# Kernel optimization log

Hardware: AMD Instinct MI355X
Metric: run time of the kernel (lower is better)

## Reference

```python
import jax, jax.numpy as jnp
import numpy as np

NUM_HEADS = 12

def setup_inputs() -> dict:
    key = jax.random.key(0)
    k1, k2, k3 = jax.random.split(key, 3)
    B, T, H = 2, 2048, 768
    x = jax.random.normal(k1, (B, T, H), dtype=jnp.float32)
    attn_mask = jnp.ones((B, T), dtype=jnp.int32)
    Wqkv = jax.random.normal(k2, (H, 3 * H), dtype=jnp.float32) * 0.02
    bqkv = jnp.zeros((3 * H,), dtype=jnp.float32)
    Wproj = jax.random.normal(k3, (H, H), dtype=jnp.float32) * 0.02
    bproj = jnp.zeros((H,), dtype=jnp.float32)
    return {"x": x, "attn_mask": attn_mask, "Wqkv": Wqkv, "bqkv": bqkv,
            "Wproj": Wproj, "bproj": bproj}

def reference(x, attn_mask, Wqkv, bqkv, Wproj, bproj):
    B, T, H = x.shape
    nh = NUM_HEADS
    hd = H // nh
    qkv = x @ Wqkv + bqkv                      # [B,T,3H]
    q, k, v = jnp.split(qkv, 3, axis=-1)
    # [B,T,H] -> [B,nh,T,hd]
    def heads(t):
        return t.reshape(B, T, nh, hd).transpose(0, 2, 1, 3)
    q, k, v = heads(q), heads(k), heads(v)
    scores = jnp.einsum('bhqd,bhkd->bhqk', q, k) / jnp.sqrt(jnp.float32(hd))
    causal = jnp.tril(jnp.ones((T, T), dtype=bool))          # allowed positions
    key_ok = attn_mask.astype(bool)[:, None, None, :]        # [B,1,1,T]
    allowed = causal[None, None] & key_ok
    scores = jnp.where(allowed, scores, -jnp.inf)
    weights = jax.nn.softmax(scores, axis=-1)                # dropout=0 (eval)
    out = jnp.einsum('bhqk,bhkd->bhqd', weights, v)
    out = out.transpose(0, 2, 1, 3).reshape(B, T, H)
    return out @ Wproj + bproj
```

## Files before the change

### kernel.cpp

```cpp
#include <hip/hip_runtime.h>
#include <stdint.h>

typedef unsigned short u16;
typedef unsigned int   u32;
typedef unsigned char  u8;
typedef __attribute__((ext_vector_type(8))) short short8;
typedef __attribute__((ext_vector_type(4))) float f32x4;
typedef __attribute__((ext_vector_type(4))) unsigned short u16x4;

#define DEV static __device__ __forceinline__

static constexpr int Bc = 2, Tc = 2048, Hc = 768, NH = 12, HD = 64;
static constexpr int BTc = Bc * Tc;
static constexpr int N3 = 3 * Hc;
static constexpr int NBH = Bc * NH;
static constexpr int NITEMS = 32 * NBH;
static constexpr float QSCALE = 0.125f * 1.44269504088896f;

DEV u16 f2bf(float f) {
  u32 u = __float_as_uint(f);
  u32 r = (u + 0x7fffu + ((u >> 16) & 1u)) >> 16;
  return (u16)r;
}

DEV float fexp2(float x) {
#if __has_builtin(__builtin_amdgcn_exp2f)
  return __builtin_amdgcn_exp2f(x);
#else
  return exp2f(x);
#endif
}

DEV u32 cvtpk_bf16(float lo, float hi) {
  u32 r;
  asm("v_cvt_pk_bf16_f32 %0, %1, %2" : "=v"(r) : "v"(lo), "v"(hi));
  return r;
}

DEV void gl_lds16(const u16* g, u16* l) {
  __builtin_amdgcn_global_load_lds(
      (const __attribute__((address_space(1))) u32*)g,
      (__attribute__((address_space(3))) u32*)l, 16, 0, 0);
}

#define MFMA(a, b, c) __builtin_amdgcn_mfma_f32_16x16x32_bf16((a), (b), (c), 0, 0, 0)

__global__ void k_cvt(const float4* __restrict__ in, uint4* __restrict__ out, int n8,
                      const int* __restrict__ mask, u8* __restrict__ flags,
                      u32* __restrict__ ctr) {
  if (blockIdx.x == 0 && threadIdx.x < 64) {
    int t = threadIdx.x;
    if (t == 0) *ctr = 0;
    int b = t >> 5, kb = t & 31;
    const int* m = mask + b * Tc + kb * 64;
    int all = 1;
    for (int i = 0; i < 64; ++i) all &= (m[i] != 0);
    flags[b * 32 + kb] = (u8)all;
  }
  int i = blockIdx.x * 256 + threadIdx.x;
  if (i >= n8) return;
  float4 a = in[2 * i], b = in[2 * i + 1];
  uint4 o;
  o.x = f2bf(a.x) | ((u32)f2bf(a.y) << 16);
  o.y = f2bf(a.z) | ((u32)f2bf(a.w) << 16);
  o.z = f2bf(b.x) | ((u32)f2bf(b.y) << 16);
  o.w = f2bf(b.z) | ((u32)f2bf(b.w) << 16);
  out[i] = o;
}

__global__ __launch_bounds__(256) void k_transpose_w(const float* __restrict__ in,
                                                     u16* __restrict__ out, int R, int C) {
  __shared__ u16 tile[64][65];
  int c0 = blockIdx.x * 64, r0 = blockIdx.y * 64;
  int tx = threadIdx.x, ty = threadIdx.y;
  for (int i = ty; i < 64; i += 4)
    tile[i][tx] = f2bf(in[(size_t)(r0 + i) * C + c0 + tx]);
  __syncthreads();
  for (int i = ty; i < 64; i += 4)
    out[(size_t)(c0 + i) * R + r0 + tx] = tile[tx][i];
}

template <int EPI>
__global__ __launch_bounds__(256) void k_gemm(const u16* __restrict__ A,
                                              const u16* __restrict__ BTm,
                                              const float* __restrict__ bias,
                                              u16* __restrict__ oQ, u16* __restrict__ oK,
                                              u16* __restrict__ oV, float* __restrict__ oF,
                                              int M, int N, int K) {
  __shared__ u16 As[128 * 32];
  __shared__ u16 Bs[128 * 32];
  const int tid = threadIdx.x;
  const int lane = tid & 63, wave = tid >> 6;
  const int wr = wave >> 1, wc = wave & 1;
  const int row0 = blockIdx.y * 128, col0 = blockIdx.x * 128;

  f32x4 acc[4][4];
#pragma unroll
  for (int m = 0; m < 4; ++m)
#pragma unroll
    for (int n = 0; n < 4; ++n) acc[m][n] = (f32x4)(0.f);

  const int srow = lane >> 2;
  const int sg = lane & 3;
  const int sf = (lane >> 3) & 3;
  const int kfetch = ((sg ^ sf) * 8);

  const int r16 = lane & 15;
  const int g = lane >> 4;
  const int fr = (r16 >> 1) & 3;
  const int koff = ((g ^ fr) * 8);

  for (int k0 = 0; k0 < K; k0 += 32) {
    if (k0) __syncthreads();
#pragma unroll
    for (int p = 0; p < 2; ++p) {
      int seg = wave * 2 + p;
      int row = seg * 16 + srow;
      gl_lds16(A + (size_t)(row0 + row) * K + k0 + kfetch, &As[seg * 512 + lane * 8]);
      gl_lds16(BTm + (size_t)(col0 + row) * K + k0 + kfetch, &Bs[seg * 512 + lane * 8]);
    }
    __syncthreads();
    short8 af[4], bf[4];
#pragma unroll
    for (int m = 0; m < 4; ++m)
      af[m] = *(const short8*)&As[(wr * 64 + m * 16 + r16) * 32 + koff];
#pragma unroll
    for (int n = 0; n < 4; ++n)
      bf[n] = *(const short8*)&Bs[(wc * 64 + n * 16 + r16) * 32 + koff];
#pragma unroll
    for (int m = 0; m < 4; ++m)
#pragma unroll
      for (int n = 0; n < 4; ++n)
        acc[m][n] = MFMA(af[m], bf[n], acc[m][n]);
  }

#pragma unroll
  for (int m = 0; m < 4; ++m) {
    int rowg = row0 + wr * 64 + m * 16 + g * 4;
#pragma unroll
    for (int n = 0; n < 4; ++n) {
      int colg = col0 + wc * 64 + n * 16 + r16;
      float bv = bias[colg];
      if constexpr (EPI == 0) {
        int which = colg / Hc;
        int hc = colg - which * Hc;
        int h = hc >> 6, d = hc & 63;
        int b = rowg >> 11, t0 = rowg & 2047;
        if (which == 2) {
          u16x4 pk;
#pragma unroll
          for (int r = 0; r < 4; ++r) pk[r] = f2bf(acc[m][n][r] + bv);
          *(u16x4*)&oV[((size_t)(b * NH + h) * HD + d) * Tc + t0] = pk;
        } else {
#pragma unroll
          for (int r = 0; r < 4; ++r) {
            float v = acc[m][n][r] + bv;
            size_t dst = ((size_t)(b * NH + h) * Tc + t0 + r) * HD + d;
            if (which == 0) oQ[dst] = f2bf(v * QSCALE);
            else            oK[dst] = f2bf(v);
          }
        }
      } else {
#pragma unroll
        for (int r = 0; r < 4; ++r)
          oF[(size_t)(rowg + r) * Hc + colg] = acc[m][n][r] + bv;
      }
    }
  }
}

__global__ __launch_bounds__(256) void k_attn(const u16* __restrict__ Qh,
                                              const u16* __restrict__ Kh,
                                              const u16* __restrict__ VT,
                                              const int* __restrict__ mask,
                                              const u8* __restrict__ flags,
                                              u16* __restrict__ O,
                                              u32* __restrict__ ctr) {
  __shared__ u16 Ks[4][4096];
  __shared__ u16 Vs[4][4096];
  __shared__ u16 Ps[4][1024];
  __shared__ int s_item;
  const int tid = threadIdx.x, lane = tid & 63, wave = tid >> 6;
  const int r16 = lane & 15, g = lane >> 4;
  const int r7 = r16 & 7;
  const int skey = lane >> 3;
  const int sgr = lane & 7;
  const int sgd = ((sgr ^ skey) * 8);

  const int off0 = r16 * 64 + ((g ^ r7) * 8);
  const int off1 = r16 * 64 + (((4 + g) ^ r7) * 8);
  const int pwb = r16 * 32 + 2 * (g & 1);
  const int pgs = g >> 1;

  for (;;) {
    if (tid == 0) s_item = (int)atomicAdd(ctr, 1u);
    __syncthreads();
    const int item = s_item;
    if (item >= NITEMS) break;
    const int qt = 31 - item / NBH;
    const int bh = item % NBH;
    const int b = bh / NH, h = bh - b * NH;
    const int q0 = qt * 64;
    const int nt = qt + 1;
    const int qg = q0 + wave * 16 + r16;
    const int* mrow = mask + b * Tc;
    const u8* frow = flags + b * 32;

    const u16* qbase = Qh + ((size_t)bh * Tc + qg) * HD;
    const short8 qf0 = *(const short8*)(qbase + g * 8);
    const short8 qf1 = *(const short8*)(qbase + 32 + g * 8);

    f32x4 acc[4];
#pragma unroll
    for (int n = 0; n < 4; ++n) acc[n] = (f32x4)(0.f);
    float mrun = -3.0e38f, lrun = 0.f;

#pragma unroll
    for (int p = 0; p < 2; ++p) {
      int seg = wave * 2 + p;
      int rloc = seg * 8 + skey;
      gl_lds16(Kh + ((size_t)bh * Tc + rloc) * HD + sgd, &Ks[0][seg * 512 + lane * 8]);
      gl_lds16(VT + ((size_t)bh * HD + rloc) * Tc + sgd, &Vs[0][seg * 512 + lane * 8]);
    }
    if (nt > 1) {
#pragma unroll
      for (int p = 0; p < 2; ++p) {
        int seg = wave * 2 + p;
        int rloc = seg * 8 + skey;
        gl_lds16(Kh + ((size_t)bh * Tc + 64 + rloc) * HD + sgd, &Ks[1][seg * 512 + lane * 8]);
        gl_lds16(VT + ((size_t)bh * HD + rloc) * Tc + 64 + sgd, &Vs[1][seg * 512 + lane * 8]);
      }
    }

    for (int t = 0; t < nt; ++t) {
      const int kb = t * 64;
      const int rem = nt - 1 - t;

      if (rem >= 2) {
        const int kb2 = kb + 128;
        const int sp = (t + 2) & 3;
#pragma unroll
        for (int p = 0; p < 2; ++p) {
          int seg = wave * 2 + p;
          int rloc = seg * 8 + skey;
          gl_lds16(Kh + ((size_t)bh * Tc + kb2 + rloc) * HD + sgd,
                   &Ks[sp][seg * 512 + lane * 8]);
          gl_lds16(VT + ((size_t)bh * HD + rloc) * Tc + kb2 + sgd,
                   &Vs[sp][seg * 512 + lane * 8]);
        }
      }

      if (rem >= 2)      asm volatile("s_waitcnt vmcnt(8)" ::: "memory");
      else if (rem == 1) asm volatile("s_waitcnt vmcnt(4)" ::: "memory");
      else               asm volatile("s_waitcnt vmcnt(0)" ::: "memory");
      __builtin_amdgcn_sched_barrier(0);
      __builtin_amdgcn_s_barrier();
      __builtin_amdgcn_sched_barrier(0);

      const u16* Kc = &Ks[t & 3][0];
      const u16* Vc = &Vs[t & 3][0];

      f32x4 s[4];
#pragma unroll
      for (int n = 0; n < 4; ++n) {
        short8 kf0 = *(const short8*)&Kc[n * 1024 + off0];
        short8 kf1 = *(const short8*)&Kc[n * 1024 + off1];
        f32x4 z = (f32x4)(0.f);
        z = MFMA(kf0, qf0, z);
        z = MFMA(kf1, qf1, z);
        s[n] = z;
      }

      const bool diag = (t == nt - 1);
      if (diag || !frow[t]) {
        const int fl = frow[t];
#pragma unroll
        for (int n = 0; n < 4; ++n)
#pragma unroll
          for (int r = 0; r < 4; ++r) {
            int keyg = kb + n * 16 + g * 4 + r;
            bool ok = fl ? true : (mrow[keyg] != 0);
            if (diag) ok = ok && (keyg <= qg);
            if (!ok) s[n][r] = -3.0e38f;
          }
      }

      float lm;
      {
        float m0 = fmaxf(fmaxf(s[0][0], s[0][1]), fmaxf(s[0][2], s[0][3]));
        float m1 = fmaxf(fmaxf(s[1][0], s[1][1]), fmaxf(s[1][2], s[1][3]));
        float m2 = fmaxf(fmaxf(s[2][0], s[2][1]), fmaxf(s[2][2], s[2][3]));
        float m3 = fmaxf(fmaxf(s[3][0], s[3][1]), fmaxf(s[3][2], s[3][3]));
        lm = fmaxf(fmaxf(m0, m1), fmaxf(m2, m3));
      }
      if (!__all(lm <= mrun + 8.0f)) {
        float rm = fmaxf(lm, __shfl_xor(lm, 16));
        rm = fmaxf(rm, __shfl_xor(rm, 32));
        float nm = fmaxf(mrun, rm);
        float alpha = fexp2(mrun - nm);
        mrun = nm;
        lrun *= alpha;
#pragma unroll
        for (int r = 0; r < 4; ++r) {
          float ar = __shfl(alpha, g * 4 + r);
          acc[0][r] *= ar;
          acc[1][r] *= ar;
          acc[2][r] *= ar;
          acc[3][r] *= ar;
        }
      }
      float rs = 0.f;
#pragma unroll
      for (int n = 0; n < 4; ++n)
#pragma unroll
        for (int r = 0; r < 4; ++r) {
          float p = fexp2(s[n][r] - mrun);
          s[n][r] = p;
          rs += p;
        }
      lrun += rs;

      u32* pw = (u32*)&Ps[wave][0];
#pragma unroll
      for (int n = 0; n < 4; ++n) {
        u32 lo = cvtpk_bf16(s[n][0], s[n][1]);
        u32 hi = cvtpk_bf16(s[n][2], s[n][3]);
        int idx = pwb + (((2 * n + pgs) ^ r7) * 4);
        *(uint2*)&pw[idx] = make_uint2(lo, hi);
      }
      asm volatile("s_waitcnt lgkmcnt(0)" ::: "memory");
      const u16* pwr = &Ps[wave][0];
      short8 pa0 = *(const short8*)&pwr[off0];
      short8 pa1 = *(const short8*)&pwr[off1];

#pragma unroll
      for (int n = 0; n < 4; ++n) {
        short8 vf0 = *(const short8*)&Vc[n * 1024 + off0];
        short8 vf1 = *(const short8*)&Vc[n * 1024 + off1];
        acc[n] = MFMA(pa0, vf0, acc[n]);
        acc[n] = MFMA(pa1, vf1, acc[n]);
      }
      __builtin_amdgcn_sched_barrier(0);
    }

    float lt = lrun + __shfl_xor(lrun, 16);
    lt += __shfl_xor(lt, 32);
#pragma unroll
    for (int r = 0; r < 4; ++r) {
      int qr = q0 + wave * 16 + g * 4 + r;
      float inv = 1.0f / __shfl(lt, g * 4 + r);
      u16* orow = O + ((size_t)(b * Tc + qr)) * Hc + h * 64;
#pragma unroll
      for (int n = 0; n < 4; ++n) orow[n * 16 + r16] = f2bf(acc[n][r] * inv);
    }
  }
}

extern "C" void kernel_launch(void* const* d_in, const int* in_sizes, int n_in,
                              void* d_out, int out_size, void* d_ws, size_t ws_size,
                              hipStream_t stream) {
  const float* x = (const float*)d_in[0];
  const int* mask = (const int*)d_in[1];
  const float* Wqkv = (const float*)d_in[2];
  const float* bqkv = (const float*)d_in[3];
  const float* Wproj = (const float*)d_in[4];
  const float* bproj = (const float*)d_in[5];
  float* out = (float*)d_out;

  char* ws = (char*)d_ws;
  size_t off = 0;
  auto alloc = [&](size_t bytes) {
    char* p = ws + off;
    off += (bytes + 255) & ~(size_t)255;
    return p;
  };
  u16* xb     = (u16*)alloc((size_t)BTc * Hc * 2);
  u16* WqkvT  = (u16*)alloc((size_t)N3 * Hc * 2);
  u16* WprojT = (u16*)alloc((size_t)Hc * Hc * 2);
  u16* Qh     = (u16*)alloc((size_t)BTc * Hc * 2);
  u16* Kh     = (u16*)alloc((size_t)BTc * Hc * 2);
  u16* VT     = (u16*)alloc((size_t)BTc * Hc * 2);
  u32* ctr    = (u32*)alloc(256);
  u8*  flags  = (u8*)alloc(256);
  u16* Ob     = xb;

  int n8 = BTc * Hc / 8;
  k_cvt<<<(n8 + 255) / 256, 256, 0, stream>>>((const float4*)x, (uint4*)xb, n8,
                                              mask, flags, ctr);
  k_transpose_w<<<dim3(N3 / 64, Hc / 64), dim3(64, 4), 0, stream>>>(Wqkv, WqkvT, Hc, N3);
  k_transpose_w<<<dim3(Hc / 64, Hc / 64), dim3(64, 4), 0, stream>>>(Wproj, WprojT, Hc, Hc);
  k_gemm<0><<<dim3(N3 / 128, BTc / 128), 256, 0, stream>>>(xb, WqkvT, bqkv, Qh, Kh, VT,
                                                           nullptr, BTc, N3, Hc);
  k_attn<<<dim3(512), 256, 0, stream>>>(Qh, Kh, VT, mask, flags, Ob, ctr);
  k_gemm<1><<<dim3(Hc / 128, BTc / 128), 256, 0, stream>>>(Ob, WprojT, bproj, nullptr,
                                                           nullptr, nullptr, out, BTc, Hc, Hc);
}
```

Before: 112.9 us.

## Split attention key tiles across wave pairs and merge partial softmax states

The attention kernel moves from 256 to 512 threads per block. Each pair of waves now shares a 16-row query group and splits every 64-key tile into two 32-key halves, each wave computing its half of the scores and PV product. At the end the two partial results (running max, sum, accumulator) are combined through shared memory. The aim is more waves in flight per block and a shorter dependent chain per wave, at the cost of an extra merge step with two barriers and more register and LDS pressure. It also adds s_setprio around the MFMA sections.

Result: faster. 107.1 us (-5.1%).

```diff
diff --git a/kernel.cpp b/kernel.cpp
--- a/kernel.cpp
+++ b/kernel.cpp
@@ -16,6 +16,8 @@
 static constexpr int NBH = Bc * NH;
 static constexpr int NITEMS = 32 * NBH;
 static constexpr float QSCALE = 0.125f * 1.44269504088896f;
+static constexpr float MRINIT = -1.0e38f;
+static constexpr float SMASK  = -3.0e38f;
 
 DEV u16 f2bf(float f) {
   u32 u = __float_as_uint(f);
@@ -169,18 +171,20 @@
   }
 }
 
-__global__ __launch_bounds__(256) void k_attn(const u16* __restrict__ Qh,
-                                              const u16* __restrict__ Kh,
-                                              const u16* __restrict__ VT,
-                                              const int* __restrict__ mask,
-                                              const u8* __restrict__ flags,
-                                              u16* __restrict__ O,
-                                              u32* __restrict__ ctr) {
+__global__ __launch_bounds__(512, 4) void k_attn(const u16* __restrict__ Qh,
+                                                 const u16* __restrict__ Kh,
+                                                 const u16* __restrict__ VT,
+                                                 const int* __restrict__ mask,
+                                                 const u8* __restrict__ flags,
+                                                 u16* __restrict__ O,
+                                                 u32* __restrict__ ctr) {
   __shared__ u16 Ks[4][4096];
   __shared__ u16 Vs[4][4096];
-  __shared__ u16 Ps[4][1024];
+  __shared__ u16 Ps[8][512];
   __shared__ int s_item;
   const int tid = threadIdx.x, lane = tid & 63, wave = tid >> 6;
+  const int qgrp = wave >> 1;
+  const int kh = wave & 1;
   const int r16 = lane & 15, g = lane >> 4;
   const int r7 = r16 & 7;
   const int skey = lane >> 3;
@@ -189,8 +193,8 @@
 
   const int off0 = r16 * 64 + ((g ^ r7) * 8);
   const int off1 = r16 * 64 + (((4 + g) ^ r7) * 8);
-  const int pwb = r16 * 32 + 2 * (g & 1);
-  const int pgs = g >> 1;
+  const int offv = kh ? off1 : off0;
+  const int prd = r16 * 16 + ((g ^ (r16 & 3)) << 2);
 
   for (;;) {
     if (tid == 0) s_item = (int)atomicAdd(ctr, 1u);
@@ -202,7 +206,7 @@
     const int b = bh / NH, h = bh - b * NH;
     const int q0 = qt * 64;
     const int nt = qt + 1;
-    const int qg = q0 + wave * 16 + r16;
+    const int qg = q0 + qgrp * 16 + r16;
     const int* mrow = mask + b * Tc;
     const u8* frow = flags + b * 32;
 
@@ -213,22 +217,15 @@
     f32x4 acc[4];
 #pragma unroll
     for (int n = 0; n < 4; ++n) acc[n] = (f32x4)(0.f);
-    float mrun = -3.0e38f, lrun = 0.f;
-
-#pragma unroll
-    for (int p = 0; p < 2; ++p) {
-      int seg = wave * 2 + p;
-      int rloc = seg * 8 + skey;
-      gl_lds16(Kh + ((size_t)bh * Tc + rloc) * HD + sgd, &Ks[0][seg * 512 + lane * 8]);
-      gl_lds16(VT + ((size_t)bh * HD + rloc) * Tc + sgd, &Vs[0][seg * 512 + lane * 8]);
-    }
-    if (nt > 1) {
-#pragma unroll
-      for (int p = 0; p < 2; ++p) {
-        int seg = wave * 2 + p;
-        int rloc = seg * 8 + skey;
-        gl_lds16(Kh + ((size_t)bh * Tc + 64 + rloc) * HD + sgd, &Ks[1][seg * 512 + lane * 8]);
-        gl_lds16(VT + ((size_t)bh * HD + rloc) * Tc + 64 + sgd, &Vs[1][seg * 512 + lane * 8]);
+    float mrun = MRINIT, lrun = 0.f;
+
+    {
+      int rloc = wave * 8 + skey;
+      gl_lds16(Kh + ((size_t)bh * Tc + rloc) * HD + sgd, &Ks[0][wave * 512 + lane * 8]);
+      gl_lds16(VT + ((size_t)bh * HD + rloc) * Tc + sgd, &Vs[0][wave * 512 + lane * 8]);
+      if (nt > 1) {
+        gl_lds16(Kh + ((size_t)bh * Tc + 64 + rloc) * HD + sgd, &Ks[1][wave * 512 + lane * 8]);
+        gl_lds16(VT + ((size_t)bh * HD + rloc) * Tc + 64 + sgd, &Vs[1][wave * 512 + lane * 8]);
       }
     }
 
@@ -239,19 +236,15 @@
       if (rem >= 2) {
         const int kb2 = kb + 128;
         const int sp = (t + 2) & 3;
-#pragma unroll
-        for (int p = 0; p < 2; ++p) {
-          int seg = wave * 2 + p;
-          int rloc = seg * 8 + skey;
-          gl_lds16(Kh + ((size_t)bh * Tc + kb2 + rloc) * HD + sgd,
-                   &Ks[sp][seg * 512 + lane * 8]);
-          gl_lds16(VT + ((size_t)bh * HD + rloc) * Tc + kb2 + sgd,
-                   &Vs[sp][seg * 512 + lane * 8]);
-        }
-      }
-
-      if (rem >= 2)      asm volatile("s_waitcnt vmcnt(8)" ::: "memory");
-      else if (rem == 1) asm volatile("s_waitcnt vmcnt(4)" ::: "memory");
+        int rloc = wave * 8 + skey;
+        gl_lds16(Kh + ((size_t)bh * Tc + kb2 + rloc) * HD + sgd,
+                 &Ks[sp][wave * 512 + lane * 8]);
+        gl_lds16(VT + ((size_t)bh * HD + rloc) * Tc + kb2 + sgd,
+                 &Vs[sp][wave * 512 + lane * 8]);
+      }
+
+      if (rem >= 2)      asm volatile("s_waitcnt vmcnt(4)" ::: "memory");
+      else if (rem == 1) asm volatile("s_waitcnt vmcnt(2)" ::: "memory");
       else               asm volatile("s_waitcnt vmcnt(0)" ::: "memory");
       __builtin_amdgcn_sched_barrier(0);
       __builtin_amdgcn_s_barrier();
@@ -260,28 +253,31 @@
       const u16* Kc = &Ks[t & 3][0];
       const u16* Vc = &Vs[t & 3][0];
 
-      f32x4 s[4];
-#pragma unroll
-      for (int n = 0; n < 4; ++n) {
-        short8 kf0 = *(const short8*)&Kc[n * 1024 + off0];
-        short8 kf1 = *(const short8*)&Kc[n * 1024 + off1];
+      f32x4 s[2];
+      __builtin_amdgcn_s_setprio(1);
+#pragma unroll
+      for (int np = 0; np < 2; ++np) {
+        const int ng = 2 * kh + np;
+        short8 kf0 = *(const short8*)&Kc[ng * 1024 + off0];
+        short8 kf1 = *(const short8*)&Kc[ng * 1024 + off1];
         f32x4 z = (f32x4)(0.f);
         z = MFMA(kf0, qf0, z);
         z = MFMA(kf1, qf1, z);
-        s[n] = z;
-      }
+        s[np] = z;
+      }
+      __builtin_amdgcn_s_setprio(0);
 
       const bool diag = (t == nt - 1);
       if (diag || !frow[t]) {
         const int fl = frow[t];
 #pragma unroll
-        for (int n = 0; n < 4; ++n)
+        for (int np = 0; np < 2; ++np)
 #pragma unroll
           for (int r = 0; r < 4; ++r) {
-            int keyg = kb + n * 16 + g * 4 + r;
+            int keyg = kb + 16 * (2 * kh + np) + 4 * g + r;
             bool ok = fl ? true : (mrow[keyg] != 0);
             if (diag) ok = ok && (keyg <= qg);
-            if (!ok) s[n][r] = -3.0e38f;
+            if (!ok) s[np][r] = SMASK;
           }
       }
 
@@ -289,9 +285,7 @@
       {
         float m0 = fmaxf(fmaxf(s[0][0], s[0][1]), fmaxf(s[0][2], s[0][3]));
         float m1 = fmaxf(fmaxf(s[1][0], s[1][1]), fmaxf(s[1][2], s[1][3]));
-        float m2 = fmaxf(fmaxf(s[2][0], s[2][1]), fmaxf(s[2][2], s[2][3]));
-        float m3 = fmaxf(fmaxf(s[3][0], s[3][1]), fmaxf(s[3][2], s[3][3]));
-        lm = fmaxf(fmaxf(m0, m1), fmaxf(m2, m3));
+        lm = fmaxf(m0, m1);
       }
       if (!__all(lm <= mrun + 8.0f)) {
         float rm = fmaxf(lm, __shfl_xor(lm, 16));
@@ -311,47 +305,74 @@
       }
       float rs = 0.f;
 #pragma unroll
-      for (int n = 0; n < 4; ++n)
+      for (int np = 0; np < 2; ++np)
 #pragma unroll
         for (int r = 0; r < 4; ++r) {
-          float p = fexp2(s[n][r] - mrun);
-          s[n][r] = p;
+          float p = fexp2(s[np][r] - mrun);
+          s[np][r] = p;
           rs += p;
         }
       lrun += rs;
 
       u32* pw = (u32*)&Ps[wave][0];
 #pragma unroll
+      for (int np = 0; np < 2; ++np) {
+        u32 lo = cvtpk_bf16(s[np][0], s[np][1]);
+        u32 hi = cvtpk_bf16(s[np][2], s[np][3]);
+        int kg = 2 * np + (g >> 1);
+        int idx = r16 * 16 + ((kg ^ (r16 & 3)) << 2) + 2 * (g & 1);
+        *(uint2*)&pw[idx] = make_uint2(lo, hi);
+      }
+      short8 pa = *(const short8*)&pw[prd];
+
+      __builtin_amdgcn_s_setprio(1);
+#pragma unroll
       for (int n = 0; n < 4; ++n) {
-        u32 lo = cvtpk_bf16(s[n][0], s[n][1]);
-        u32 hi = cvtpk_bf16(s[n][2], s[n][3]);
-        int idx = pwb + (((2 * n + pgs) ^ r7) * 4);
-        *(uint2*)&pw[idx] = make_uint2(lo, hi);
-      }
-      asm volatile("s_waitcnt lgkmcnt(0)" ::: "memory");
-      const u16* pwr = &Ps[wave][0];
-      short8 pa0 = *(const short8*)&pwr[off0];
-      short8 pa1 = *(const short8*)&pwr[off1];
-
-#pragma unroll
-      for (int n = 0; n < 4; ++n) {
-        short8 vf0 = *(const short8*)&Vc[n * 1024 + off0];
-        short8 vf1 = *(const short8*)&Vc[n * 1024 + off1];
-        acc[n] = MFMA(pa0, vf0, acc[n]);
-        acc[n] = MFMA(pa1, vf1, acc[n]);
-      }
+        short8 vf = *(const short8*)&Vc[n * 1024 + offv];
+        acc[n] = MFMA(pa, vf, acc[n]);
+      }
+      __builtin_amdgcn_s_setprio(0);
       __builtin_amdgcn_sched_barrier(0);
     }
 
     float lt = lrun + __shfl_xor(lrun, 16);
     lt += __shfl_xor(lt, 32);
-#pragma unroll
-    for (int r = 0; r < 4; ++r) {
-      int qr = q0 + wave * 16 + g * 4 + r;
-      float inv = 1.0f / __shfl(lt, g * 4 + r);
-      u16* orow = O + ((size_t)(b * Tc + qr)) * Hc + h * 64;
-#pragma unroll
-      for (int n = 0; n < 4; ++n) orow[n * 16 + r16] = f2bf(acc[n][r] * inv);
+
+    __syncthreads();
+    float* ab = (float*)&Ks[0][0] + qgrp * 1024;
+    float* ml = (float*)&Ps[0][0];
+    if (kh == 1) {
+#pragma unroll
+      for (int n = 0; n < 4; ++n)
+#pragma unroll
+        for (int r = 0; r < 4; ++r)
+          ab[(4 * g + r) * 64 + 16 * n + r16] = acc[n][r];
+      if (g == 0) {
+        ml[qgrp * 32 + r16 * 2]     = mrun;
+        ml[qgrp * 32 + r16 * 2 + 1] = lt;
+      }
+    }
+    __syncthreads();
+    if (kh == 0) {
+#pragma unroll
+      for (int r = 0; r < 4; ++r) {
+        int q = 4 * g + r;
+        float mA = __shfl(mrun, q);
+        float lA = __shfl(lt, q);
+        float mB = ml[qgrp * 32 + q * 2];
+        float lB = ml[qgrp * 32 + q * 2 + 1];
+        float ms = fmaxf(mA, mB);
+        float cA = fexp2(mA - ms);
+        float cB = fexp2(mB - ms);
+        float linv = 1.0f / (lA * cA + lB * cB);
+        int qr = q0 + qgrp * 16 + q;
+        u16* orow = O + ((size_t)(b * Tc + qr)) * Hc + h * 64;
+#pragma unroll
+        for (int n = 0; n < 4; ++n) {
+          float v = (acc[n][r] * cA + ab[q * 64 + 16 * n + r16] * cB) * linv;
+          orow[n * 16 + r16] = f2bf(v);
+        }
+      }
     }
   }
 }
@@ -391,7 +412,7 @@
   k_transpose_w<<<dim3(Hc / 64, Hc / 64), dim3(64, 4), 0, stream>>>(Wproj, WprojT, Hc, Hc);
   k_gemm<0><<<dim3(N3 / 128, BTc / 128), 256, 0, stream>>>(xb, WqkvT, bqkv, Qh, Kh, VT,
                                                            nullptr, BTc, N3, Hc);
-  k_attn<<<dim3(512), 256, 0, stream>>>(Qh, Kh, VT, mask, flags, Ob, ctr);
+  k_attn<<<dim3(512), 512, 0, stream>>>(Qh, Kh, VT, mask, flags, Ob, ctr);
   k_gemm<1><<<dim3(Hc / 128, BTc / 128), 256, 0, stream>>>(Ob, WprojT, bproj, nullptr,
                                                            nullptr, nullptr, out, BTc, Hc, Hc);
 }
```
